# Performance work log

Measured on AMD Instinct MI355X. Metric: run time of the kernel, lower is better.

Reference implementation:

```python
import jax, jax.numpy as jnp
import numpy as np

N_HEADS = 8
HEAD_DIM = 64  # d_model // n_heads = 512 // 8


def setup_inputs() -> dict:
    key = jax.random.key(0)
    kq, kk, kv, km = jax.random.split(key, 4)
    B, C, H, L, D = 8, 4, N_HEADS, 512, HEAD_DIM
    q = jax.random.normal(kq, (B * C, H, L, D), dtype=jnp.float32)
    k = jax.random.normal(kk, (B * C, H, D, L), dtype=jnp.float32)  # pre-transposed, matmul(q, k) directly
    v = jax.random.normal(kv, (B * C, H, L, D), dtype=jnp.float32)
    attn_mask = jax.random.randint(km, (B, L, L), 0, 2).astype(bool)  # True = masked out
    return {"q": q, "k": k, "v": v, "attn_mask": attn_mask}


def reference(q, k, v, attn_mask):
    # q: [B*C, H, L, D]; k: [B*C, H, D, L]; v: [B*C, H, L, D]; attn_mask: [B, L, L] bool
    scale = jnp.asarray(HEAD_DIM ** (-0.5), dtype=q.dtype)
    scores = jnp.einsum('ghld,ghdm->ghlm', q, k) * scale  # [B*C, H, L, L]
    if attn_mask is not None:
        B = attn_mask.shape[0]
        C = q.shape[0] // B
        H, L = scores.shape[1], scores.shape[2]
        scores = scores.reshape(B, C, H, L, L)
        mask = attn_mask[:, None, None, :, :]  # broadcast over channels and heads
        scores = jnp.where(mask, -jnp.inf, scores)
        scores = scores.reshape(B * C, H, L, L)
    attn_weights = jax.nn.softmax(scores, axis=-1)  # dropout p=0.0 -> identity (eval)
    output = jnp.einsum('ghlm,ghmd->ghld', attn_weights, v)  # [B*C, H, L, D]
    return output
```

## Files before the change

kernel.cpp:

```cpp
#include <hip/hip_runtime.h>


typedef __attribute__((ext_vector_type(8)))  short bf16x8;
typedef __attribute__((ext_vector_type(16))) float f32x16;

union Frag4 { uint4 x; unsigned u[4]; bf16x8 v; };

__device__ __forceinline__ unsigned pk_bf16(float a, float b){
    unsigned ua = __builtin_bit_cast(unsigned, a) + 0x8000u;
    unsigned ub = __builtin_bit_cast(unsigned, b) + 0x8000u;
    return __builtin_amdgcn_perm(ub, ua, 0x07060302u);
}

__device__ __forceinline__ float fast_exp2(float x){
#if __has_builtin(__builtin_amdgcn_exp2f)
    return __builtin_amdgcn_exp2f(x);
#else
    return exp2f(x);
#endif
}

#define L2E 1.44269504088896f

__global__ __launch_bounds__(256)
void pack_mask(const int* __restrict__ mg, unsigned long long* __restrict__ bits)
{
    const int t    = blockIdx.x*256 + threadIdx.x;
    const int lane = t & 63;
    const int w0   = t >> 6;
    const int strd = (int)((gridDim.x*256) >> 6);
    const int nW   = 8*512*8;
    for (int i = w0; i < nW; i += strd){
        int v = mg[(size_t)i*64 + lane];
        unsigned long long m = __ballot(v != 0);
        if (lane == 0) bits[i] = m;
    }
}

#define STAGE_LOAD(kbx, kf, vf)                                               \
    {                                                                         \
        _Pragma("unroll")                                                     \
        for (int gi=0; gi<2; ++gi){                                           \
            const float* kp_ = kh + (size_t)((wv + gi*4)*8)*512 + (kbx)*64 + lane; \
            _Pragma("unroll")                                                 \
            for (int dd=0; dd<8; ++dd) kf[gi*8+dd] = kp_[(size_t)dd*512];     \
            const float* vp_ = vh + (size_t)((kbx)*64 + (wv + gi*4)*8)*64 + lane;  \
            _Pragma("unroll")                                                 \
            for (int mm=0; mm<8; ++mm) vf[gi*8+mm] = vp_[(size_t)mm*64];      \
        }                                                                     \
    }

#define STAGE_WRITE(buf, kf, vf)                                              \
    {                                                                         \
        _Pragma("unroll")                                                     \
        for (int gi=0; gi<2; ++gi){                                           \
            const int g_ = wv + gi*4;                                         \
            Frag4 wk_;                                                        \
            wk_.u[0]=pk_bf16(kf[gi*8+0],kf[gi*8+1]);                          \
            wk_.u[1]=pk_bf16(kf[gi*8+2],kf[gi*8+3]);                          \
            wk_.u[2]=pk_bf16(kf[gi*8+4],kf[gi*8+5]);                          \
            wk_.u[3]=pk_bf16(kf[gi*8+6],kf[gi*8+7]);                          \
            sKt4[buf][lane*8 + (g_ ^ (lane&7))] = wk_.x;                      \
            Frag4 wv_;                                                        \
            wv_.u[0]=pk_bf16(vf[gi*8+0],vf[gi*8+1]);                          \
            wv_.u[1]=pk_bf16(vf[gi*8+2],vf[gi*8+3]);                          \
            wv_.u[2]=pk_bf16(vf[gi*8+4],vf[gi*8+5]);                          \
            wv_.u[3]=pk_bf16(vf[gi*8+6],vf[gi*8+7]);                          \
            sVt4[buf][lane*8 + (g_ ^ (lane&7))] = wv_.x;                      \
        }                                                                     \
    }

template<int BITS>
__global__ __launch_bounds__(256, 4)
void attn_fused(const float* __restrict__ qg, const float* __restrict__ kg,
                const float* __restrict__ vg, const int* __restrict__ mg,
                const unsigned* __restrict__ bits, float* __restrict__ og)
{
    __shared__ uint4 sKt4[2][64*8];
    __shared__ uint4 sVt4[2][64*8];

    const int t    = threadIdx.x;
    const int lane = t & 63;
    const int wv   = t >> 6;
    const int col  = lane & 31;
    const int h    = lane >> 5;

    const int bi   = blockIdx.x;
    const int s    = bi >> 3;
    const int head = (bi & 7)*32 + (s >> 2);
    const int qt   = s & 3;
    const int b    = bi & 7;

    const float* qh = qg + (size_t)head*32768;
    const float* kh = kg + (size_t)head*32768;
    const float* vh = vg + (size_t)head*32768;
    float*       oh = og + (size_t)head*32768;

    const int qrl = wv*32 + col;
    const int* mrow0 = BITS ? nullptr
        : mg + (size_t)b*262144 + (size_t)(qt*128 + qrl)*512;
    const unsigned* brow = BITS
        ? bits + ((size_t)b*512 + qt*128 + qrl)*16
        : nullptr;

    Frag4 qf[4];
    {
        const float* qr = qh + (size_t)(qt*128 + qrl)*64 + h*8;
        #pragma unroll
        for (int kt=0; kt<4; ++kt){
            float4 x0 = *(const float4*)(qr + kt*16);
            float4 x1 = *(const float4*)(qr + kt*16 + 4);
            qf[kt].u[0] = pk_bf16(x0.x*0.125f, x0.y*0.125f);
            qf[kt].u[1] = pk_bf16(x0.z*0.125f, x0.w*0.125f);
            qf[kt].u[2] = pk_bf16(x1.x*0.125f, x1.y*0.125f);
            qf[kt].u[3] = pk_bf16(x1.z*0.125f, x1.w*0.125f);
        }
    }

    f32x16 o0, o1;
    #pragma unroll
    for (int i=0;i<16;++i){ o0[i]=0.f; o1[i]=0.f; }
    float lsum = 0.f;

    {
        float k0[16], v0[16];
        STAGE_LOAD(0, k0, v0);
        STAGE_WRITE(0, k0, v0);
    }
    __syncthreads();

    for (int kb=0; kb<8; ++kb){
        const int cur = kb & 1;
        const int nx  = (kb+1) & 7;

        uint2 mbv;
        if constexpr (BITS) mbv = *(const uint2*)(brow + kb*2);
        float kn[16], vn[16];
        STAGE_LOAD(nx, kn, vn);
        __builtin_amdgcn_sched_barrier(0);

        #pragma unroll
        for (int mt=0; mt<2; ++mt){
            f32x16 sc;
            #pragma unroll
            for (int i=0;i<16;++i) sc[i]=0.f;
            __builtin_amdgcn_s_setprio(1);
            #pragma unroll
            for (int kt=0; kt<4; ++kt){
                const int r = mt*32 + col;
                Frag4 a; a.x = sKt4[cur][r*8 + ((kt*2+h) ^ (r&7))];
                sc = __builtin_amdgcn_mfma_f32_32x32x16_bf16(a.v, qf[kt].v, sc, 0, 0, 0);
            }
            __builtin_amdgcn_s_setprio(0);

            unsigned pp[8];
            if constexpr (BITS){
                const unsigned mword = mt ? mbv.y : mbv.x;
                #pragma unroll
                for (int rg=0; rg<4; ++rg){
                    const unsigned mw = mword >> (rg*8 + h*4);
                    float e0 = (mw & 1u) ? 0.f : fast_exp2(sc[4*rg+0]*L2E);
                    float e1 = (mw & 2u) ? 0.f : fast_exp2(sc[4*rg+1]*L2E);
                    float e2 = (mw & 4u) ? 0.f : fast_exp2(sc[4*rg+2]*L2E);
                    float e3 = (mw & 8u) ? 0.f : fast_exp2(sc[4*rg+3]*L2E);
                    lsum += (e0+e1)+(e2+e3);
                    pp[2*rg]   = pk_bf16(e0, e1);
                    pp[2*rg+1] = pk_bf16(e2, e3);
                }
            } else {
                const int* mrow = mrow0 + kb*64;
                #pragma unroll
                for (int rg=0; rg<4; ++rg){
                    int4 mm = *(const int4*)(mrow + mt*32 + rg*8 + h*4);
                    float e0 = mm.x ? 0.f : fast_exp2(sc[4*rg+0]*L2E);
                    float e1 = mm.y ? 0.f : fast_exp2(sc[4*rg+1]*L2E);
                    float e2 = mm.z ? 0.f : fast_exp2(sc[4*rg+2]*L2E);
                    float e3 = mm.w ? 0.f : fast_exp2(sc[4*rg+3]*L2E);
                    lsum += (e0+e1)+(e2+e3);
                    pp[2*rg]   = pk_bf16(e0, e1);
                    pp[2*rg+1] = pk_bf16(e2, e3);
                }
            }

            #pragma unroll
            for (int c=0; c<2; ++c){
                unsigned keep0 = h ? pp[4*c+2] : pp[4*c+0];
                unsigned keep1 = h ? pp[4*c+3] : pp[4*c+1];
                unsigned give0 = h ? pp[4*c+0] : pp[4*c+2];
                unsigned give1 = h ? pp[4*c+1] : pp[4*c+3];
                unsigned got0 = (unsigned)__shfl_xor((int)give0, 32, 64);
                unsigned got1 = (unsigned)__shfl_xor((int)give1, 32, 64);
                Frag4 pa;
                pa.u[0] = h ? got0  : keep0;
                pa.u[1] = h ? got1  : keep1;
                pa.u[2] = h ? keep0 : got0;
                pa.u[3] = h ? keep1 : got1;
                const int gm = mt*4 + c*2 + h;
                Frag4 b0; b0.x = sVt4[cur][col*8      + (gm ^ (col&7))];
                Frag4 b1; b1.x = sVt4[cur][(32+col)*8 + (gm ^ ((32+col)&7))];
                __builtin_amdgcn_s_setprio(1);
                o0 = __builtin_amdgcn_mfma_f32_32x32x16_bf16(pa.v, b0.v, o0, 0, 0, 0);
                o1 = __builtin_amdgcn_mfma_f32_32x32x16_bf16(pa.v, b1.v, o1, 0, 0, 0);
                __builtin_amdgcn_s_setprio(0);
            }
        }

        __builtin_amdgcn_sched_barrier(0);
        STAGE_WRITE(cur^1, kn, vn);
        __syncthreads();
    }

    lsum += __shfl_xor(lsum, 32, 64);
    const float inv = 1.0f / lsum;
    float* ob = oh + (size_t)(qt*128 + wv*32)*64;
    #pragma unroll
    for (int r=0; r<16; ++r){
        const int qq = (r&3) + 8*(r>>2) + 4*h;
        const float iv = __shfl(inv, qq, 64);
        ob[(size_t)qq*64 + col]      = o0[r]*iv;
        ob[(size_t)qq*64 + 32 + col] = o1[r]*iv;
    }
}

extern "C" void kernel_launch(void* const* d_in, const int* in_sizes, int n_in,
                              void* d_out, int out_size, void* d_ws, size_t ws_size,
                              hipStream_t stream) {
    (void)in_sizes; (void)n_in; (void)out_size;
    const float* q = (const float*)d_in[0];
    const float* k = (const float*)d_in[1];
    const float* v = (const float*)d_in[2];
    const int*   m = (const int*)d_in[3];
    const size_t BITS_BYTES = (size_t)8*512*64;
    if (d_ws && ws_size >= BITS_BYTES){
        pack_mask<<<dim3(1024), dim3(256), 0, stream>>>(m, (unsigned long long*)d_ws);
        attn_fused<1><<<dim3(1024), dim3(256), 0, stream>>>(
            q, k, v, m, (const unsigned*)d_ws, (float*)d_out);
    } else {
        attn_fused<0><<<dim3(1024), dim3(256), 0, stream>>>(
            q, k, v, m, nullptr, (float*)d_out);
    }
}
```

Measured before the change: 198.0 us.

## Split K and V prefetch across the two score halves to cut register pressure

The next block's K and V prefetch is no longer issued together. K is loaded before the first 32-column half and written to LDS after it, while V is loaded after that write and stored after the second half. This halves the live prefetch registers (16 floats instead of 32), which can reduce spills or allow higher occupancy. The non-bitmask mask path is also changed to build a mask word up front so both paths share one compute body. The risk is that each load now has only half an iteration of compute to hide its latency.

```diff
diff --git a/kernel.cpp b/kernel.cpp
--- a/kernel.cpp
+++ b/kernel.cpp
@@ -37,20 +37,39 @@
     }
 }
 
-#define STAGE_LOAD(kbx, kf, vf)                                               \
+__device__ __forceinline__ unsigned build_mword(const int* p, int h){
+    unsigned w = 0;
+    #pragma unroll
+    for (int rg=0; rg<4; ++rg){
+        int4 mm = *(const int4*)(p + rg*8 + h*4);
+        const unsigned base = rg*8 + h*4;
+        w |= (mm.x?1u:0u) << base;
+        w |= (mm.y?1u:0u) << (base+1);
+        w |= (mm.z?1u:0u) << (base+2);
+        w |= (mm.w?1u:0u) << (base+3);
+    }
+    return w;
+}
+
+#define LOADK(kbx, kf)                                                        \
     {                                                                         \
         _Pragma("unroll")                                                     \
         for (int gi=0; gi<2; ++gi){                                           \
             const float* kp_ = kh + (size_t)((wv + gi*4)*8)*512 + (kbx)*64 + lane; \
             _Pragma("unroll")                                                 \
             for (int dd=0; dd<8; ++dd) kf[gi*8+dd] = kp_[(size_t)dd*512];     \
+        }                                                                     \
+    }
+#define LOADV(kbx, vf)                                                        \
+    {                                                                         \
+        _Pragma("unroll")                                                     \
+        for (int gi=0; gi<2; ++gi){                                           \
             const float* vp_ = vh + (size_t)((kbx)*64 + (wv + gi*4)*8)*64 + lane;  \
             _Pragma("unroll")                                                 \
             for (int mm=0; mm<8; ++mm) vf[gi*8+mm] = vp_[(size_t)mm*64];      \
         }                                                                     \
     }
-
-#define STAGE_WRITE(buf, kf, vf)                                              \
+#define WRITEK(buf, kf)                                                       \
     {                                                                         \
         _Pragma("unroll")                                                     \
         for (int gi=0; gi<2; ++gi){                                           \
@@ -61,12 +80,67 @@
             wk_.u[2]=pk_bf16(kf[gi*8+4],kf[gi*8+5]);                          \
             wk_.u[3]=pk_bf16(kf[gi*8+6],kf[gi*8+7]);                          \
             sKt4[buf][lane*8 + (g_ ^ (lane&7))] = wk_.x;                      \
+        }                                                                     \
+    }
+#define WRITEV(buf, vf)                                                       \
+    {                                                                         \
+        _Pragma("unroll")                                                     \
+        for (int gi=0; gi<2; ++gi){                                           \
+            const int g_ = wv + gi*4;                                         \
             Frag4 wv_;                                                        \
             wv_.u[0]=pk_bf16(vf[gi*8+0],vf[gi*8+1]);                          \
             wv_.u[1]=pk_bf16(vf[gi*8+2],vf[gi*8+3]);                          \
             wv_.u[2]=pk_bf16(vf[gi*8+4],vf[gi*8+5]);                          \
             wv_.u[3]=pk_bf16(vf[gi*8+6],vf[gi*8+7]);                          \
             sVt4[buf][lane*8 + (g_ ^ (lane&7))] = wv_.x;                      \
+        }                                                                     \
+    }
+
+#define MT_BODY(mt, mword)                                                    \
+    {                                                                         \
+        f32x16 sc;                                                            \
+        _Pragma("unroll")                                                     \
+        for (int i=0;i<16;++i) sc[i]=0.f;                                     \
+        __builtin_amdgcn_s_setprio(1);                                        \
+        _Pragma("unroll")                                                     \
+        for (int kt=0; kt<4; ++kt){                                           \
+            const int r = (mt)*32 + col;                                      \
+            Frag4 a; a.x = sKt4[cur][r*8 + ((kt*2+h) ^ (r&7))];               \
+            sc = __builtin_amdgcn_mfma_f32_32x32x16_bf16(a.v, qf[kt].v, sc, 0, 0, 0); \
+        }                                                                     \
+        __builtin_amdgcn_s_setprio(0);                                        \
+        unsigned pp[8];                                                       \
+        _Pragma("unroll")                                                     \
+        for (int rg=0; rg<4; ++rg){                                           \
+            const unsigned mw = (mword) >> (rg*8 + h*4);                      \
+            float e0 = (mw & 1u) ? 0.f : fast_exp2(sc[4*rg+0]*L2E);           \
+            float e1 = (mw & 2u) ? 0.f : fast_exp2(sc[4*rg+1]*L2E);           \
+            float e2 = (mw & 4u) ? 0.f : fast_exp2(sc[4*rg+2]*L2E);           \
+            float e3 = (mw & 8u) ? 0.f : fast_exp2(sc[4*rg+3]*L2E);           \
+            lsum += (e0+e1)+(e2+e3);                                          \
+            pp[2*rg]   = pk_bf16(e0, e1);                                     \
+            pp[2*rg+1] = pk_bf16(e2, e3);                                     \
+        }                                                                     \
+        _Pragma("unroll")                                                     \
+        for (int c=0; c<2; ++c){                                              \
+            unsigned keep0 = h ? pp[4*c+2] : pp[4*c+0];                       \
+            unsigned keep1 = h ? pp[4*c+3] : pp[4*c+1];                       \
+            unsigned give0 = h ? pp[4*c+0] : pp[4*c+2];                       \
+            unsigned give1 = h ? pp[4*c+1] : pp[4*c+3];                       \
+            unsigned got0 = (unsigned)__shfl_xor((int)give0, 32, 64);         \
+            unsigned got1 = (unsigned)__shfl_xor((int)give1, 32, 64);         \
+            Frag4 pa;                                                         \
+            pa.u[0] = h ? got0  : keep0;      \
+            pa.u[1] = h ? got1  : keep1;                    \
+            pa.u[2] = h ? keep0 : got0;       \
+            pa.u[3] = h ? keep1 : got1;                     \
+            const int gm = (mt)*4 + c*2 + h;  \
+            Frag4 b0; b0.x = sVt4[cur][col*8      + (gm ^ (col&7))];          \
+            Frag4 b1; b1.x = sVt4[cur][(32+col)*8 + (gm ^ ((32+col)&7))];     \
+            __builtin_amdgcn_s_setprio(1);                                    \
+            o0 = __builtin_amdgcn_mfma_f32_32x32x16_bf16(pa.v, b0.v, o0, 0, 0, 0); \
+            o1 = __builtin_amdgcn_mfma_f32_32x32x16_bf16(pa.v, b1.v, o1, 0, 0, 0); \
+            __builtin_amdgcn_s_setprio(0);                                    \
         }                                                                     \
     }
 
@@ -123,90 +197,45 @@
     float lsum = 0.f;
 
     {
-        float k0[16], v0[16];
-        STAGE_LOAD(0, k0, v0);
-        STAGE_WRITE(0, k0, v0);
+        float k0[16];
+        LOADK(0, k0); WRITEK(0, k0);
+    }
+    {
+        float v0[16];
+        LOADV(0, v0); WRITEV(0, v0);
     }
     __syncthreads();
 
     for (int kb=0; kb<8; ++kb){
         const int cur = kb & 1;
-        const int nx  = (kb+1) & 7;
-
-        uint2 mbv;
-        if constexpr (BITS) mbv = *(const uint2*)(brow + kb*2);
-        float kn[16], vn[16];
-        STAGE_LOAD(nx, kn, vn);
-        __builtin_amdgcn_sched_barrier(0);
-
-        #pragma unroll
-        for (int mt=0; mt<2; ++mt){
-            f32x16 sc;
-            #pragma unroll
-            for (int i=0;i<16;++i) sc[i]=0.f;
-            __builtin_amdgcn_s_setprio(1);
-            #pragma unroll
-            for (int kt=0; kt<4; ++kt){
-                const int r = mt*32 + col;
-                Frag4 a; a.x = sKt4[cur][r*8 + ((kt*2+h) ^ (r&7))];
-                sc = __builtin_amdgcn_mfma_f32_32x32x16_bf16(a.v, qf[kt].v, sc, 0, 0, 0);
-            }
-            __builtin_amdgcn_s_setprio(0);
-
-            unsigned pp[8];
-            if constexpr (BITS){
-                const unsigned mword = mt ? mbv.y : mbv.x;
-                #pragma unroll
-                for (int rg=0; rg<4; ++rg){
-                    const unsigned mw = mword >> (rg*8 + h*4);
-                    float e0 = (mw & 1u) ? 0.f : fast_exp2(sc[4*rg+0]*L2E);
-                    float e1 = (mw & 2u) ? 0.f : fast_exp2(sc[4*rg+1]*L2E);
-                    float e2 = (mw & 4u) ? 0.f : fast_exp2(sc[4*rg+2]*L2E);
-                    float e3 = (mw & 8u) ? 0.f : fast_exp2(sc[4*rg+3]*L2E);
-                    lsum += (e0+e1)+(e2+e3);
-                    pp[2*rg]   = pk_bf16(e0, e1);
-                    pp[2*rg+1] = pk_bf16(e2, e3);
-                }
-            } else {
-                const int* mrow = mrow0 + kb*64;
-                #pragma unroll
-                for (int rg=0; rg<4; ++rg){
-                    int4 mm = *(const int4*)(mrow + mt*32 + rg*8 + h*4);
-                    float e0 = mm.x ? 0.f : fast_exp2(sc[4*rg+0]*L2E);
-                    float e1 = mm.y ? 0.f : fast_exp2(sc[4*rg+1]*L2E);
-                    float e2 = mm.z ? 0.f : fast_exp2(sc[4*rg+2]*L2E);
-                    float e3 = mm.w ? 0.f : fast_exp2(sc[4*rg+3]*L2E);
-                    lsum += (e0+e1)+(e2+e3);
-                    pp[2*rg]   = pk_bf16(e0, e1);
-                    pp[2*rg+1] = pk_bf16(e2, e3);
-                }
-            }
-
-            #pragma unroll
-            for (int c=0; c<2; ++c){
-                unsigned keep0 = h ? pp[4*c+2] : pp[4*c+0];
-                unsigned keep1 = h ? pp[4*c+3] : pp[4*c+1];
-                unsigned give0 = h ? pp[4*c+0] : pp[4*c+2];
-                unsigned give1 = h ? pp[4*c+1] : pp[4*c+3];
-                unsigned got0 = (unsigned)__shfl_xor((int)give0, 32, 64);
-                unsigned got1 = (unsigned)__shfl_xor((int)give1, 32, 64);
-                Frag4 pa;
-                pa.u[0] = h ? got0  : keep0;
-                pa.u[1] = h ? got1  : keep1;
-                pa.u[2] = h ? keep0 : got0;
-                pa.u[3] = h ? keep1 : got1;
-                const int gm = mt*4 + c*2 + h;
-                Frag4 b0; b0.x = sVt4[cur][col*8      + (gm ^ (col&7))];
-                Frag4 b1; b1.x = sVt4[cur][(32+col)*8 + (gm ^ ((32+col)&7))];
-                __builtin_amdgcn_s_setprio(1);
-                o0 = __builtin_amdgcn_mfma_f32_32x32x16_bf16(pa.v, b0.v, o0, 0, 0, 0);
-                o1 = __builtin_amdgcn_mfma_f32_32x32x16_bf16(pa.v, b1.v, o1, 0, 0, 0);
-                __builtin_amdgcn_s_setprio(0);
-            }
+        const int nxb = cur ^ 1;
+        const int nx  = (kb < 7) ? kb+1 : 7;
+
+        unsigned mword0, mword1;
+        if constexpr (BITS){
+            uint2 mbv = *(const uint2*)(brow + kb*2);
+            mword0 = mbv.x; mword1 = mbv.y;
+        } else {
+            mword0 = build_mword(mrow0 + kb*64,      h);
+            mword1 = build_mword(mrow0 + kb*64 + 32, h);
         }
 
-        __builtin_amdgcn_sched_barrier(0);
-        STAGE_WRITE(cur^1, kn, vn);
+        float kn[16];
+        LOADK(nx, kn);
+        __builtin_amdgcn_sched_barrier(0);
+
+        MT_BODY(0, mword0)
+
+        __builtin_amdgcn_sched_barrier(0);
+        WRITEK(nxb, kn);
+        float vn[16];
+        LOADV(nx, vn);
+        __builtin_amdgcn_sched_barrier(0);
+
+        MT_BODY(1, mword1)
+
+        __builtin_amdgcn_sched_barrier(0);
+        WRITEV(nxb, vn);
         __syncthreads();
     }
 
```

Measured after the change: 176.5 us. 1.12x faster.

## Process two 32-row query groups per wave to reuse K/V tiles

Applied to the files above, without the earlier changes.

Each wave now handles 64 query rows (two 32-row groups), so every block covers 256 queries and the grid is halved. K and V tiles staged in LDS, and the K fragments read from LDS, are reused across both query groups, which halves global K/V loads and LDS staging per query. The cost is higher register pressure (four output accumulators, two score tiles), reflected in the relaxed launch bounds. Fewer blocks means lower occupancy and fewer waves to hide latency.

```diff
diff --git a/kernel.cpp b/kernel.cpp
--- a/kernel.cpp
+++ b/kernel.cpp
@@ -37,20 +37,39 @@
     }
 }
 
-#define STAGE_LOAD(kbx, kf, vf)                                               \
+__device__ __forceinline__ unsigned build_mword(const int* p, int h){
+    unsigned w = 0;
+    #pragma unroll
+    for (int rg=0; rg<4; ++rg){
+        int4 mm = *(const int4*)(p + rg*8 + h*4);
+        const unsigned base = rg*8 + h*4;
+        w |= (mm.x?1u:0u) << base;
+        w |= (mm.y?1u:0u) << (base+1);
+        w |= (mm.z?1u:0u) << (base+2);
+        w |= (mm.w?1u:0u) << (base+3);
+    }
+    return w;
+}
+
+#define LOADK(kbx, kf)                                                        \
     {                                                                         \
         _Pragma("unroll")                                                     \
         for (int gi=0; gi<2; ++gi){                                           \
             const float* kp_ = kh + (size_t)((wv + gi*4)*8)*512 + (kbx)*64 + lane; \
             _Pragma("unroll")                                                 \
             for (int dd=0; dd<8; ++dd) kf[gi*8+dd] = kp_[(size_t)dd*512];     \
+        }                                                                     \
+    }
+#define LOADV(kbx, vf)                                                        \
+    {                                                                         \
+        _Pragma("unroll")                                                     \
+        for (int gi=0; gi<2; ++gi){                                           \
             const float* vp_ = vh + (size_t)((kbx)*64 + (wv + gi*4)*8)*64 + lane;  \
             _Pragma("unroll")                                                 \
             for (int mm=0; mm<8; ++mm) vf[gi*8+mm] = vp_[(size_t)mm*64];      \
         }                                                                     \
     }
-
-#define STAGE_WRITE(buf, kf, vf)                                              \
+#define WRITEK(buf, kf)                                                       \
     {                                                                         \
         _Pragma("unroll")                                                     \
         for (int gi=0; gi<2; ++gi){                                           \
@@ -61,6 +80,13 @@
             wk_.u[2]=pk_bf16(kf[gi*8+4],kf[gi*8+5]);                          \
             wk_.u[3]=pk_bf16(kf[gi*8+6],kf[gi*8+7]);                          \
             sKt4[buf][lane*8 + (g_ ^ (lane&7))] = wk_.x;                      \
+        }                                                                     \
+    }
+#define WRITEV(buf, vf)                                                       \
+    {                                                                         \
+        _Pragma("unroll")                                                     \
+        for (int gi=0; gi<2; ++gi){                                           \
+            const int g_ = wv + gi*4;                                         \
             Frag4 wv_;                                                        \
             wv_.u[0]=pk_bf16(vf[gi*8+0],vf[gi*8+1]);                          \
             wv_.u[1]=pk_bf16(vf[gi*8+2],vf[gi*8+3]);                          \
@@ -71,7 +97,7 @@
     }
 
 template<int BITS>
-__global__ __launch_bounds__(256, 4)
+__global__ __launch_bounds__(256, 2)
 void attn_fused(const float* __restrict__ qg, const float* __restrict__ kg,
                 const float* __restrict__ vg, const int* __restrict__ mg,
                 const unsigned* __restrict__ bits, float* __restrict__ og)
@@ -87,8 +113,8 @@
 
     const int bi   = blockIdx.x;
     const int s    = bi >> 3;
-    const int head = (bi & 7)*32 + (s >> 2);
-    const int qt   = s & 3;
+    const int head = (bi & 7)*32 + (s >> 1);
+    const int qt   = s & 1;
     const int b    = bi & 7;
 
     const float* qh = qg + (size_t)head*32768;
@@ -96,129 +122,153 @@
     const float* vh = vg + (size_t)head*32768;
     float*       oh = og + (size_t)head*32768;
 
-    const int qrl = wv*32 + col;
-    const int* mrow0 = BITS ? nullptr
-        : mg + (size_t)b*262144 + (size_t)(qt*128 + qrl)*512;
-    const unsigned* brow = BITS
-        ? bits + ((size_t)b*512 + qt*128 + qrl)*16
-        : nullptr;
-
-    Frag4 qf[4];
-    {
-        const float* qr = qh + (size_t)(qt*128 + qrl)*64 + h*8;
+    const int qr0 = qt*256 + wv*64 + col;
+    const int qr1 = qr0 + 32;
+    const int* mrow0 = BITS ? nullptr : mg + (size_t)b*262144 + (size_t)qr0*512;
+    const int* mrow1 = BITS ? nullptr : mg + (size_t)b*262144 + (size_t)qr1*512;
+    const unsigned* brow0 = BITS ? bits + ((size_t)b*512 + qr0)*16 : nullptr;
+    const unsigned* brow1 = BITS ? bits + ((size_t)b*512 + qr1)*16 : nullptr;
+
+    Frag4 qf[2][4];
+    #pragma unroll
+    for (int cg=0; cg<2; ++cg){
+        const float* qr = qh + (size_t)(cg ? qr1 : qr0)*64 + h*8;
         #pragma unroll
         for (int kt=0; kt<4; ++kt){
             float4 x0 = *(const float4*)(qr + kt*16);
             float4 x1 = *(const float4*)(qr + kt*16 + 4);
-            qf[kt].u[0] = pk_bf16(x0.x*0.125f, x0.y*0.125f);
-            qf[kt].u[1] = pk_bf16(x0.z*0.125f, x0.w*0.125f);
-            qf[kt].u[2] = pk_bf16(x1.x*0.125f, x1.y*0.125f);
-            qf[kt].u[3] = pk_bf16(x1.z*0.125f, x1.w*0.125f);
+            qf[cg][kt].u[0] = pk_bf16(x0.x*0.125f, x0.y*0.125f);
+            qf[cg][kt].u[1] = pk_bf16(x0.z*0.125f, x0.w*0.125f);
+            qf[cg][kt].u[2] = pk_bf16(x1.x*0.125f, x1.y*0.125f);
+            qf[cg][kt].u[3] = pk_bf16(x1.z*0.125f, x1.w*0.125f);
         }
     }
 
-    f32x16 o0, o1;
-    #pragma unroll
-    for (int i=0;i<16;++i){ o0[i]=0.f; o1[i]=0.f; }
-    float lsum = 0.f;
+    f32x16 o[2][2];
+    #pragma unroll
+    for (int cg=0; cg<2; ++cg)
+        #pragma unroll
+        for (int dk=0; dk<2; ++dk)
+            #pragma unroll
+            for (int i=0;i<16;++i) o[cg][dk][i]=0.f;
+    float ls[2] = {0.f, 0.f};
 
     {
-        float k0[16], v0[16];
-        STAGE_LOAD(0, k0, v0);
-        STAGE_WRITE(0, k0, v0);
+        float k0[16];
+        LOADK(0, k0); WRITEK(0, k0);
+    }
+    {
+        float v0[16];
+        LOADV(0, v0); WRITEV(0, v0);
     }
     __syncthreads();
 
     for (int kb=0; kb<8; ++kb){
         const int cur = kb & 1;
-        const int nx  = (kb+1) & 7;
-
-        uint2 mbv;
-        if constexpr (BITS) mbv = *(const uint2*)(brow + kb*2);
+        const int nxb = cur ^ 1;
+        const int nx  = (kb < 7) ? kb+1 : 7;
+
+        uint2 mb[2];
+        if constexpr (BITS){
+            mb[0] = *(const uint2*)(brow0 + kb*2);
+            mb[1] = *(const uint2*)(brow1 + kb*2);
+        } else {
+            mb[0].x = build_mword(mrow0 + kb*64,      h);
+            mb[0].y = build_mword(mrow0 + kb*64 + 32, h);
+            mb[1].x = build_mword(mrow1 + kb*64,      h);
+            mb[1].y = build_mword(mrow1 + kb*64 + 32, h);
+        }
         float kn[16], vn[16];
-        STAGE_LOAD(nx, kn, vn);
+        LOADK(nx, kn);
+        LOADV(nx, vn);
         __builtin_amdgcn_sched_barrier(0);
 
         #pragma unroll
         for (int mt=0; mt<2; ++mt){
-            f32x16 sc;
-            #pragma unroll
-            for (int i=0;i<16;++i) sc[i]=0.f;
-            __builtin_amdgcn_s_setprio(1);
+            Frag4 a[4];
             #pragma unroll
             for (int kt=0; kt<4; ++kt){
                 const int r = mt*32 + col;
-                Frag4 a; a.x = sKt4[cur][r*8 + ((kt*2+h) ^ (r&7))];
-                sc = __builtin_amdgcn_mfma_f32_32x32x16_bf16(a.v, qf[kt].v, sc, 0, 0, 0);
+                a[kt].x = sKt4[cur][r*8 + ((kt*2+h) ^ (r&7))];
+            }
+            f32x16 sc[2];
+            #pragma unroll
+            for (int cg=0; cg<2; ++cg)
+                #pragma unroll
+                for (int i=0;i<16;++i) sc[cg][i]=0.f;
+            __builtin_amdgcn_s_setprio(1);
+            #pragma unroll
+            for (int kt=0; kt<4; ++kt){
+                sc[0] = __builtin_amdgcn_mfma_f32_32x32x16_bf16(a[kt].v, qf[0][kt].v, sc[0], 0, 0, 0);
+                sc[1] = __builtin_amdgcn_mfma_f32_32x32x16_bf16(a[kt].v, qf[1][kt].v, sc[1], 0, 0, 0);
             }
             __builtin_amdgcn_s_setprio(0);
 
-            unsigned pp[8];
-            if constexpr (BITS){
-                const unsigned mword = mt ? mbv.y : mbv.x;
+            unsigned pp[2][8];
+            #pragma unroll
+            for (int cg=0; cg<2; ++cg){
+                const unsigned mword = mt ? mb[cg].y : mb[cg].x;
                 #pragma unroll
                 for (int rg=0; rg<4; ++rg){
                     const unsigned mw = mword >> (rg*8 + h*4);
-                    float e0 = (mw & 1u) ? 0.f : fast_exp2(sc[4*rg+0]*L2E);
-                    float e1 = (mw & 2u) ? 0.f : fast_exp2(sc[4*rg+1]*L2E);
-                    float e2 = (mw & 4u) ? 0.f : fast_exp2(sc[4*rg+2]*L2E);
-                    float e3 = (mw & 8u) ? 0.f : fast_exp2(sc[4*rg+3]*L2E);
-                    lsum += (e0+e1)+(e2+e3);
-                    pp[2*rg]   = pk_bf16(e0, e1);
-                    pp[2*rg+1] = pk_bf16(e2, e3);
+                    float e0 = (mw & 1u) ? 0.f : fast_exp2(sc[cg][4*rg+0]*L2E);
+                    float e1 = (mw & 2u) ? 0.f : fast_exp2(sc[cg][4*rg+1]*L2E);
+                    float e2 = (mw & 4u) ? 0.f : fast_exp2(sc[cg][4*rg+2]*L2E);
+                    float e3 = (mw & 8u) ? 0.f : fast_exp2(sc[cg][4*rg+3]*L2E);
+                    ls[cg] += (e0+e1)+(e2+e3);
+                    pp[cg][2*rg]   = pk_bf16(e0, e1);
+                    pp[cg][2*rg+1] = pk_bf16(e2, e3);
                 }
-            } else {
-                const int* mrow = mrow0 + kb*64;
+            }
+
+            #pragma unroll
+            for (int c=0; c<2; ++c){
+                Frag4 pa[2];
                 #pragma unroll
-                for (int rg=0; rg<4; ++rg){
-                    int4 mm = *(const int4*)(mrow + mt*32 + rg*8 + h*4);
-                    float e0 = mm.x ? 0.f : fast_exp2(sc[4*rg+0]*L2E);
-                    float e1 = mm.y ? 0.f : fast_exp2(sc[4*rg+1]*L2E);
-                    float e2 = mm.z ? 0.f : fast_exp2(sc[4*rg+2]*L2E);
-                    float e3 = mm.w ? 0.f : fast_exp2(sc[4*rg+3]*L2E);
-                    lsum += (e0+e1)+(e2+e3);
-                    pp[2*rg]   = pk_bf16(e0, e1);
-                    pp[2*rg+1] = pk_bf16(e2, e3);
+                for (int cg=0; cg<2; ++cg){
+                    unsigned keep0 = h ? pp[cg][4*c+2] : pp[cg][4*c+0];
+                    unsigned keep1 = h ? pp[cg][4*c+3] : pp[cg][4*c+1];
+                    unsigned give0 = h ? pp[cg][4*c+0] : pp[cg][4*c+2];
+                    unsigned give1 = h ? pp[cg][4*c+1] : pp[cg][4*c+3];
+                    unsigned got0 = (unsigned)__shfl_xor((int)give0, 32, 64);
+                    unsigned got1 = (unsigned)__shfl_xor((int)give1, 32, 64);
+                    pa[cg].u[0] = h ? got0  : keep0;
+                    pa[cg].u[1] = h ? got1  : keep1;
+                    pa[cg].u[2] = h ? keep0 : got0;
+                    pa[cg].u[3] = h ? keep1 : got1;
                 }
-            }
-
-            #pragma unroll
-            for (int c=0; c<2; ++c){
-                unsigned keep0 = h ? pp[4*c+2] : pp[4*c+0];
-                unsigned keep1 = h ? pp[4*c+3] : pp[4*c+1];
-                unsigned give0 = h ? pp[4*c+0] : pp[4*c+2];
-                unsigned give1 = h ? pp[4*c+1] : pp[4*c+3];
-                unsigned got0 = (unsigned)__shfl_xor((int)give0, 32, 64);
-                unsigned got1 = (unsigned)__shfl_xor((int)give1, 32, 64);
-                Frag4 pa;
-                pa.u[0] = h ? got0  : keep0;
-                pa.u[1] = h ? got1  : keep1;
-                pa.u[2] = h ? keep0 : got0;
-                pa.u[3] = h ? keep1 : got1;
                 const int gm = mt*4 + c*2 + h;
                 Frag4 b0; b0.x = sVt4[cur][col*8      + (gm ^ (col&7))];
                 Frag4 b1; b1.x = sVt4[cur][(32+col)*8 + (gm ^ ((32+col)&7))];
                 __builtin_amdgcn_s_setprio(1);
-                o0 = __builtin_amdgcn_mfma_f32_32x32x16_bf16(pa.v, b0.v, o0, 0, 0, 0);
-                o1 = __builtin_amdgcn_mfma_f32_32x32x16_bf16(pa.v, b1.v, o1, 0, 0, 0);
+                o[0][0] = __builtin_amdgcn_mfma_f32_32x32x16_bf16(pa[0].v, b0.v, o[0][0], 0, 0, 0);
+                o[0][1] = __builtin_amdgcn_mfma_f32_32x32x16_bf16(pa[0].v, b1.v, o[0][1], 0, 0, 0);
+                o[1][0] = __builtin_amdgcn_mfma_f32_32x32x16_bf16(pa[1].v, b0.v, o[1][0], 0, 0, 0);
+                o[1][1] = __builtin_amdgcn_mfma_f32_32x32x16_bf16(pa[1].v, b1.v, o[1][1], 0, 0, 0);
                 __builtin_amdgcn_s_setprio(0);
             }
         }
 
         __builtin_amdgcn_sched_barrier(0);
-        STAGE_WRITE(cur^1, kn, vn);
+        WRITEK(nxb, kn);
+        WRITEV(nxb, vn);
         __syncthreads();
     }
 
-    lsum += __shfl_xor(lsum, 32, 64);
-    const float inv = 1.0f / lsum;
-    float* ob = oh + (size_t)(qt*128 + wv*32)*64;
+    ls[0] += __shfl_xor(ls[0], 32, 64);
+    ls[1] += __shfl_xor(ls[1], 32, 64);
+    const float inv0 = 1.0f / ls[0];
+    const float inv1 = 1.0f / ls[1];
+    float* ob = oh + (size_t)(qt*256 + wv*64)*64;
     #pragma unroll
     for (int r=0; r<16; ++r){
         const int qq = (r&3) + 8*(r>>2) + 4*h;
-        const float iv = __shfl(inv, qq, 64);
-        ob[(size_t)qq*64 + col]      = o0[r]*iv;
-        ob[(size_t)qq*64 + 32 + col] = o1[r]*iv;
+        const float iv0 = __shfl(inv0, qq, 64);
+        const float iv1 = __shfl(inv1, qq, 64);
+        ob[(size_t)qq*64      + col]      = o[0][0][r]*iv0;
+        ob[(size_t)qq*64      + 32 + col] = o[0][1][r]*iv0;
+        ob[(size_t)(32+qq)*64 + col]      = o[1][0][r]*iv1;
+        ob[(size_t)(32+qq)*64 + 32 + col] = o[1][1][r]*iv1;
     }
 }
 
@@ -233,10 +283,10 @@
     const size_t BITS_BYTES = (size_t)8*512*64;
     if (d_ws && ws_size >= BITS_BYTES){
         pack_mask<<<dim3(1024), dim3(256), 0, stream>>>(m, (unsigned long long*)d_ws);
-        attn_fused<1><<<dim3(1024), dim3(256), 0, stream>>>(
+        attn_fused<1><<<dim3(512), dim3(256), 0, stream>>>(
             q, k, v, m, (const unsigned*)d_ws, (float*)d_out);
     } else {
-        attn_fused<0><<<dim3(1024), dim3(256), 0, stream>>>(
+        attn_fused<0><<<dim3(512), dim3(256), 0, stream>>>(
             q, k, v, m, nullptr, (float*)d_out);
     }
 }
```

After: 183.3 us. -7.4%, faster.
